# Kernel tuning notes

Hardware: AMD Instinct MI355X
Metric: run time of the kernel (lower is better)

The kernel has to match this reference:

```python
import jax, jax.numpy as jnp
import numpy as np

NF, NLOC, NNEI = 4, 2048, 64
EMBED, PAIR_DIM, H = 128, 64, 8
HD = EMBED // H
EPS = 1e-5

def _ln(x, g, b):
    m = x.mean(-1, keepdims=True)
    v = ((x - m) ** 2).mean(-1, keepdims=True)
    return (x - m) * jax.lax.rsqrt(v + EPS) * g + b

def setup_inputs() -> dict:
    key = jax.random.key(0)
    ks = jax.random.split(key, 12)
    inp = {
        "query": jax.random.normal(ks[0], (NF, NLOC, EMBED), jnp.float32),
        "pair": jax.random.normal(ks[1], (NF, NLOC, NNEI, PAIR_DIM), jnp.float32),
        "nlist": jax.random.randint(ks[2], (NF, NLOC, NNEI), 0, NLOC, jnp.int64),
        "delta_pos": jax.random.normal(ks[3], (NF, NLOC, NNEI, 3), jnp.float32),
        "attn_mask": jnp.zeros((NF, H, NLOC, NNEI), jnp.float32),
        "ln_g": jnp.ones((EMBED,), jnp.float32),
        "ln_b": jnp.zeros((EMBED,), jnp.float32),
        "pn_g": jnp.ones((PAIR_DIM,), jnp.float32),
        "pn_b": jnp.zeros((PAIR_DIM,), jnp.float32),
        "Wq": jax.random.normal(ks[4], (EMBED, EMBED), jnp.float32) * (EMBED ** -0.5),
        "Wk": jax.random.normal(ks[5], (EMBED, EMBED), jnp.float32) * (EMBED ** -0.5),
        "Wv": jax.random.normal(ks[6], (EMBED, EMBED), jnp.float32) * (EMBED ** -0.5),
        "Wbias": jax.random.normal(ks[7], (H, PAIR_DIM), jnp.float32) * (PAIR_DIM ** -0.5),
        "bbias": jnp.zeros((H,), jnp.float32),
        "Wforce": jax.random.normal(ks[8], (1, EMBED), jnp.float32) * (EMBED ** -0.5),
    }
    return inp

def reference(query, pair, nlist, delta_pos, attn_mask,
              ln_g, ln_b, pn_g, pn_b, Wq, Wk, Wv, Wbias, bbias, Wforce):
    nf, nloc, _ = query.shape
    nnei = nlist.shape[-1]
    qn = _ln(query, ln_g, ln_b)            # [f,l,e]
    pn = _ln(pair, pn_g, pn_b)             # [f,l,n,p]
    scaling = HD ** -0.5
    q = (qn @ Wq.T).reshape(nf, nloc, H, HD) * scaling       # [f,l,h,d]
    k = qn @ Wk.T                                            # [f,l,e]
    v = qn @ Wv.T
    idx = nlist.reshape(nf, -1)[..., None]                   # [f,l*n,1]
    kg = jnp.take_along_axis(k, idx, axis=1).reshape(nf, nloc, nnei, H, HD)
    vg = jnp.take_along_axis(v, idx, axis=1).reshape(nf, nloc, nnei, H, HD)
    attn = jnp.einsum('flhd,flnhd->fhln', q, kg)             # [f,h,l,n]
    bias = jnp.einsum('flnp,hp->fhln', pn, Wbias) + bbias[None, :, None, None]
    probs = jax.nn.softmax(attn + attn_mask + bias, axis=-1)  # dropout off (eval)
    # rotate by delta_pos and contract with v over neighbors
    x = jnp.einsum('fhln,flnc,flnhd->flchd', probs, delta_pos, vg)
    x = x.reshape(nf, nloc, 3, EMBED)
    force = (x @ Wforce.T).squeeze(-1)                       # [f,l,3]
    return force
```

## Files before the change

### kernel.cpp

```cpp
#include <hip/hip_runtime.h>

#define NFR   4
#define NLOCC 2048
#define NNEIN 64
#define EMB   128
#define PDIM  64
#define NH    8
#define LNEPS 1e-5f
#define NROW  (NFR*NLOCC)

#define WS_Q   0
#define WS_K   (NROW*EMB)
#define WS_FV  (2*NROW*EMB)
#define WS_WVF (2*NROW*EMB + NROW*NH)
#define WS_G   (WS_WVF + NH*EMB)
#define WS_SG  (WS_G + NH*PDIM)

__device__ __forceinline__ void fma4(float4& acc, const float4 a, const float4 b) {
    acc.x = fmaf(a.x, b.x, acc.x);
    acc.y = fmaf(a.y, b.y, acc.y);
    acc.z = fmaf(a.z, b.z, acc.z);
    acc.w = fmaf(a.w, b.w, acc.w);
}
__device__ __forceinline__ void fma4s(float4& acc, const float s, const float4 b) {
    acc.x = fmaf(s, b.x, acc.x);
    acc.y = fmaf(s, b.y, acc.y);
    acc.z = fmaf(s, b.z, acc.z);
    acc.w = fmaf(s, b.w, acc.w);
}
__device__ __forceinline__ float hsum4(const float4 a) {
    return (a.x + a.y) + (a.z + a.w);
}
__device__ __forceinline__ float dot4(const float4 a, const float4 b) {
    return fmaf(a.x, b.x, fmaf(a.y, b.y, fmaf(a.z, b.z, a.w * b.w)));
}
__device__ __forceinline__ float4 scale4(const float4 a, const float s) {
    return make_float4(a.x*s, a.y*s, a.z*s, a.w*s);
}

__global__ __launch_bounds__(256) void precompute_kernel(
    const float* __restrict__ pn_g, const float* __restrict__ pn_b,
    const float* __restrict__ Wbias, const float* __restrict__ bbias,
    const float* __restrict__ Wv, const float* __restrict__ Wforce,
    float* __restrict__ ws)
{
    const int t = threadIdx.x;
    {
        const int h  = t >> 5;
        const int e0 = (t & 31) * 4;
        float4 acc = make_float4(0.f, 0.f, 0.f, 0.f);
        #pragma unroll
        for (int d = 0; d < 16; ++d) {
            const float wf = Wforce[h*16 + d];
            const float4 wv = *(const float4*)(Wv + (size_t)(h*16 + d)*EMB + e0);
            fma4s(acc, wf, wv);
        }
        *(float4*)(ws + WS_WVF + (size_t)h*EMB + e0) = acc;
    }
    for (int idx = t; idx < NH*PDIM; idx += 256) {
        const int h = idx >> 6, p = idx & 63;
        ws[WS_G + idx] = pn_g[p] * Wbias[h*PDIM + p];
    }
    if (t < NH) {
        float sg = 0.f, c = 0.f;
        #pragma unroll 8
        for (int p = 0; p < PDIM; ++p) {
            const float wb = Wbias[t*PDIM + p];
            sg = fmaf(pn_g[p], wb, sg);
            c  = fmaf(pn_b[p], wb, c);
        }
        ws[WS_SG + t]      = sg;
        ws[WS_SG + NH + t] = c + bbias[t];
    }
}

__global__ __launch_bounds__(256, 2) void qkfv_kernel(
    const float* __restrict__ query,
    const float* __restrict__ ln_g, const float* __restrict__ ln_b,
    const float* __restrict__ Wq, const float* __restrict__ Wk,
    float* __restrict__ ws)
{
    __shared__ float gb_s[2][EMB];
    __shared__ float qn_s[16*132];
    __shared__ float wt_s[2][16*132];
    const int t = threadIdx.x;
    const int rowbase = blockIdx.x * 16;

    if (t < 64) {
        const float* src = (t < 32) ? ln_g : ln_b;
        ((float4*)gb_s[t >> 5])[t & 31] = ((const float4*)src)[t & 31];
    }

    const int r   = t >> 4;
    const int seg = t & 15;
    float4 x0 = ((const float4*)query)[(size_t)(rowbase + r)*32 + seg*2 + 0];
    float4 x1 = ((const float4*)query)[(size_t)(rowbase + r)*32 + seg*2 + 1];
    float s  = (x0.x + x0.y) + (x0.z + x0.w) + (x1.x + x1.y) + (x1.z + x1.w);
    float ss = x0.x*x0.x + x0.y*x0.y + x0.z*x0.z + x0.w*x0.w
             + x1.x*x1.x + x1.y*x1.y + x1.z*x1.z + x1.w*x1.w;
    #pragma unroll
    for (int m = 1; m < 16; m <<= 1) {
        s  += __shfl_xor(s,  m, 64);
        ss += __shfl_xor(ss, m, 64);
    }
    const float mean = s * (1.0f / 128.0f);
    const float var  = ss * (1.0f / 128.0f) - mean * mean;
    const float rstd = rsqrtf(var + LNEPS);
    __syncthreads();

    {
        const int c0 = seg * 8;
        float4 o0, o1;
        o0.x = (x0.x - mean)*rstd*gb_s[0][c0+0] + gb_s[1][c0+0];
        o0.y = (x0.y - mean)*rstd*gb_s[0][c0+1] + gb_s[1][c0+1];
        o0.z = (x0.z - mean)*rstd*gb_s[0][c0+2] + gb_s[1][c0+2];
        o0.w = (x0.w - mean)*rstd*gb_s[0][c0+3] + gb_s[1][c0+3];
        o1.x = (x1.x - mean)*rstd*gb_s[0][c0+4] + gb_s[1][c0+4];
        o1.y = (x1.y - mean)*rstd*gb_s[0][c0+5] + gb_s[1][c0+5];
        o1.z = (x1.z - mean)*rstd*gb_s[0][c0+6] + gb_s[1][c0+6];
        o1.w = (x1.w - mean)*rstd*gb_s[0][c0+7] + gb_s[1][c0+7];
        ((float4*)qn_s)[r*33 + seg*2 + 0] = o0;
        ((float4*)qn_s)[r*33 + seg*2 + 1] = o1;
    }
    __syncthreads();

    const int rp = t >> 5;
    const int r0 = rp * 2;
    const int cq = t & 31;
    const int sc0 = t >> 2;
    const int si0 = t & 3;
    const float4* qn4 = (const float4*)qn_s;

    for (int w = 0; w < 2; ++w) {
        const float4* W4 = (const float4*)((w == 0) ? Wq : Wk);
        float4 acc0 = make_float4(0.f,0.f,0.f,0.f);
        float4 acc1 = make_float4(0.f,0.f,0.f,0.f);
        {
            float4 g0 = W4[(size_t)sc0*32 + si0];
            float4 g1 = W4[(size_t)(sc0+64)*32 + si0];
            float* wt = wt_s[0];
            wt[(si0*4+0)*132 + sc0] = g0.x; wt[(si0*4+1)*132 + sc0] = g0.y;
            wt[(si0*4+2)*132 + sc0] = g0.z; wt[(si0*4+3)*132 + sc0] = g0.w;
            wt[(si0*4+0)*132 + sc0+64] = g1.x; wt[(si0*4+1)*132 + sc0+64] = g1.y;
            wt[(si0*4+2)*132 + sc0+64] = g1.z; wt[(si0*4+3)*132 + sc0+64] = g1.w;
        }
        __syncthreads();
        #pragma unroll
        for (int tau = 0; tau < 8; ++tau) {
            const int buf = tau & 1;
            float4 ng0, ng1;
            if (tau < 7) {
                ng0 = W4[(size_t)sc0*32 + (tau+1)*4 + si0];
                ng1 = W4[(size_t)(sc0+64)*32 + (tau+1)*4 + si0];
            }
            const float4* wt4 = (const float4*)wt_s[buf];
            #pragma unroll
            for (int e4 = 0; e4 < 4; ++e4) {
                float4 a0 = qn4[r0*33 + tau*4 + e4];
                float4 a1 = qn4[(r0+1)*33 + tau*4 + e4];
                const float* a0p = (const float*)&a0;
                const float* a1p = (const float*)&a1;
                #pragma unroll
                for (int ee = 0; ee < 4; ++ee) {
                    const float4 wv = wt4[(e4*4+ee)*33 + cq];
                    fma4s(acc0, a0p[ee], wv);
                    fma4s(acc1, a1p[ee], wv);
                }
            }
            if (tau < 7) {
                float* wt = wt_s[buf ^ 1];
                wt[(si0*4+0)*132 + sc0] = ng0.x; wt[(si0*4+1)*132 + sc0] = ng0.y;
                wt[(si0*4+2)*132 + sc0] = ng0.z; wt[(si0*4+3)*132 + sc0] = ng0.w;
                wt[(si0*4+0)*132 + sc0+64] = ng1.x; wt[(si0*4+1)*132 + sc0+64] = ng1.y;
                wt[(si0*4+2)*132 + sc0+64] = ng1.z; wt[(si0*4+3)*132 + sc0+64] = ng1.w;
            }
            __syncthreads();
        }
        const float sc = (w == 0) ? 0.25f : 1.0f;
        float4* dst = (float4*)(ws + (w == 0 ? WS_Q : WS_K));
        dst[(size_t)(rowbase + r0)*32 + cq]     = scale4(acc0, sc);
        dst[(size_t)(rowbase + r0 + 1)*32 + cq] = scale4(acc1, sc);
    }

    if (t < 128) {
        const int rr = t >> 3, h = t & 7;
        const float4* wvf4 = (const float4*)(ws + WS_WVF + (size_t)h*EMB);
        float4 acc = make_float4(0.f,0.f,0.f,0.f);
        #pragma unroll
        for (int ch = 0; ch < 32; ++ch)
            fma4(acc, qn4[rr*33 + ch], wvf4[ch]);
        ws[WS_FV + (size_t)(rowbase + rr)*NH + h] = hsum4(acc);
    }
}

__global__ __launch_bounds__(256, 4) void attn_force_kernel(
    const float* __restrict__ pair, const int* __restrict__ nlist,
    const float* __restrict__ delta_pos, const float* __restrict__ attn_mask,
    const float* __restrict__ ws, float* __restrict__ out)
{
    __shared__ float  logit_s[NNEIN*9];
    __shared__ float4 G_s4[128];
    __shared__ float  fpart[4][3];

    const int t    = threadIdx.x;
    const int bid  = blockIdx.x;
    const int fr   = bid >> 11;
    const int l    = bid & 2047;
    const int w    = t >> 6;
    const int lane = t & 63;
    const int half = lane >> 5;
    const int c    = lane & 31;
    const int n    = (w << 4) | (lane >> 2);
    const int sub  = lane & 3;
    const int h0   = sub * 2, h1 = h0 + 1;
    const int i32  = lane & 31;
    const int hh   = (w << 1) | half;

    const float4* prow = (const float4*)(pair + ((size_t)bid*NNEIN + n)*PDIM);
    float4 pr0 = prow[sub*4+0];
    float4 pr1 = prow[sub*4+1];
    float4 pr2 = prow[sub*4+2];
    float4 pr3 = prow[sub*4+3];

    const int jv = nlist[(size_t)bid*NNEIN + lane];
    const float4 q4c = ((const float4*)(ws + WS_Q))[(size_t)bid*32 + c];

    const float mask0 = attn_mask[((size_t)(fr*NH + h0)*NLOCC + l)*NNEIN + n];
    const float mask1 = attn_mask[((size_t)(fr*NH + h1)*NLOCC + l)*NNEIN + n];
    const float sg0 = ws[WS_SG + h0],      sg1 = ws[WS_SG + h1];
    const float cc0 = ws[WS_SG + NH + h0], cc1 = ws[WS_SG + NH + h1];

    const float* dpA = delta_pos + ((size_t)bid*NNEIN + i32)*3;
    const float* dpB = delta_pos + ((size_t)bid*NNEIN + i32 + 32)*3;
    const float dpax = dpA[0], dpay = dpA[1], dpaz = dpA[2];
    const float dpbx = dpB[0], dpby = dpB[1], dpbz = dpB[2];

    if (t < 128) G_s4[t] = ((const float4*)(ws + WS_G))[t];

    const int jA = __shfl(jv, i32, 64);
    const int jB = __shfl(jv, i32 + 32, 64);
    const float fvA = ws[WS_FV + ((size_t)(fr << 11) + jA)*NH + hh];
    const float fvB = ws[WS_FV + ((size_t)(fr << 11) + jB)*NH + hh];

    {
        const float4* k4 = (const float4*)(ws + WS_K) + (size_t)(fr << 11)*32;
        int jr[8];
        #pragma unroll
        for (int i = 0; i < 8; ++i)
            jr[i] = __shfl(jv, (w << 4) | (i << 1) | half, 64);
        float4 kkA[4], kkB[4];
        #pragma unroll
        for (int i = 0; i < 4; ++i) kkA[i] = k4[(size_t)jr[i]*32 + c];
        #pragma unroll
        for (int i = 0; i < 4; ++i) kkB[i] = k4[(size_t)jr[4+i]*32 + c];
        float p[8];
        #pragma unroll
        for (int i = 0; i < 4; ++i) p[i]     = dot4(kkA[i], q4c);
        #pragma unroll
        for (int i = 0; i < 4; ++i) p[4 + i] = dot4(kkB[i], q4c);
        #pragma unroll
        for (int i = 0; i < 8; ++i) {
            float pp = p[i];
            pp += __shfl_xor(pp, 1, 64);
            pp += __shfl_xor(pp, 2, 64);
            if ((c & 3) == 0)
                logit_s[((w << 4) | (i << 1) | half)*9 + (c >> 2)] = pp;
        }
    }
    __syncthreads();

    {
        float s  = hsum4(pr0) + hsum4(pr1) + hsum4(pr2) + hsum4(pr3);
        float ss = dot4(pr0, pr0) + dot4(pr1, pr1) + dot4(pr2, pr2) + dot4(pr3, pr3);
        s  += __shfl_xor(s, 1, 64);  s  += __shfl_xor(s, 2, 64);
        ss += __shfl_xor(ss, 1, 64); ss += __shfl_xor(ss, 2, 64);
        const float mean = s * (1.0f / 64.0f);
        const float var  = ss * (1.0f / 64.0f) - mean * mean;
        const float rstd = rsqrtf(var + LNEPS);

        float d[NH];
        #pragma unroll
        for (int h = 0; h < NH; ++h) d[h] = 0.f;
        const float4 prq[4] = {pr0, pr1, pr2, pr3};
        #pragma unroll
        for (int q = 0; q < 4; ++q) {
            #pragma unroll
            for (int h = 0; h < NH; ++h)
                d[h] += dot4(prq[q], G_s4[h*16 + sub*4 + q]);
        }
        #pragma unroll
        for (int h = 0; h < NH; ++h) {
            d[h] += __shfl_xor(d[h], 1, 64);
            d[h] += __shfl_xor(d[h], 2, 64);
        }
        const float b0 = rstd*(d[h0] - mean*sg0) + cc0 + mask0;
        const float b1 = rstd*(d[h1] - mean*sg1) + cc1 + mask1;
        logit_s[n*9 + h0] += b0;
        logit_s[n*9 + h1] += b1;
    }
    __syncthreads();

    {
        float a = logit_s[i32*9 + hh], b = logit_s[(i32 + 32)*9 + hh];
        float m = fmaxf(a, b);
        #pragma unroll
        for (int mm = 16; mm >= 1; mm >>= 1) m = fmaxf(m, __shfl_xor(m, mm, 64));
        float ea = __expf(a - m), eb = __expf(b - m);
        float sum = ea + eb;
        #pragma unroll
        for (int mm = 16; mm >= 1; mm >>= 1) sum += __shfl_xor(sum, mm, 64);
        const float inv = 1.0f / sum;
        float ca = ea * inv * fvA;
        float cb = eb * inv * fvB;
        ca += __shfl_xor(ca, 32, 64);
        cb += __shfl_xor(cb, 32, 64);
        float f0 = ca*dpax + cb*dpbx;
        float f1 = ca*dpay + cb*dpby;
        float f2 = ca*dpaz + cb*dpbz;
        #pragma unroll
        for (int mm = 1; mm <= 16; mm <<= 1) {
            f0 += __shfl_xor(f0, mm, 64);
            f1 += __shfl_xor(f1, mm, 64);
            f2 += __shfl_xor(f2, mm, 64);
        }
        if (lane == 0) {
            fpart[w][0] = f0; fpart[w][1] = f1; fpart[w][2] = f2;
        }
    }
    __syncthreads();

    if (t < 3)
        out[(size_t)bid*3 + t] = fpart[0][t] + fpart[1][t] + fpart[2][t] + fpart[3][t];
}

extern "C" void kernel_launch(void* const* d_in, const int* in_sizes, int n_in,
                              void* d_out, int out_size, void* d_ws, size_t ws_size,
                              hipStream_t stream) {
    const float* query     = (const float*)d_in[0];
    const float* pair      = (const float*)d_in[1];
    const int*   nlist     = (const int*)d_in[2];
    const float* delta_pos = (const float*)d_in[3];
    const float* attn_mask = (const float*)d_in[4];
    const float* ln_g      = (const float*)d_in[5];
    const float* ln_b      = (const float*)d_in[6];
    const float* pn_g      = (const float*)d_in[7];
    const float* pn_b      = (const float*)d_in[8];
    const float* Wq        = (const float*)d_in[9];
    const float* Wk        = (const float*)d_in[10];
    const float* Wv        = (const float*)d_in[11];
    const float* Wbias     = (const float*)d_in[12];
    const float* bbias     = (const float*)d_in[13];
    const float* Wforce    = (const float*)d_in[14];
    float* out = (float*)d_out;
    float* ws  = (float*)d_ws;

    precompute_kernel<<<1, 256, 0, stream>>>(pn_g, pn_b, Wbias, bbias, Wv, Wforce, ws);
    qkfv_kernel<<<512, 256, 0, stream>>>(query, ln_g, ln_b, Wq, Wk, ws);
    attn_force_kernel<<<NROW, 256, 0, stream>>>(pair, nlist, delta_pos, attn_mask, ws, out);
}
```

Baseline: 265.2 us.

## Stage pair rows and delta_pos through LDS with coalesced loads, restructure force reduction

Pair rows are now loaded with fully coalesced float4 reads across the whole block into a padded shared-memory tile, instead of strided per-thread row loads. delta_pos is staged in shared memory, and the value gather is done as one float2 per thread. Softmax probabilities are written back to LDS and the force reduction is remapped per neighbour, which costs an extra barrier. Shared-memory use grows by about 17 KB per block, which may reduce occupancy under launch_bounds(256,4).

```diff
diff --git a/kernel.cpp b/kernel.cpp
--- a/kernel.cpp
+++ b/kernel.cpp
@@ -198,8 +198,10 @@
     const float* __restrict__ delta_pos, const float* __restrict__ attn_mask,
     const float* __restrict__ ws, float* __restrict__ out)
 {
+    __shared__ float4 pair_s4[64*17];
     __shared__ float  logit_s[NNEIN*9];
     __shared__ float4 G_s4[128];
+    __shared__ float  dp_s[192];
     __shared__ float  fpart[4][3];
 
     const int t    = threadIdx.x;
@@ -210,18 +212,21 @@
     const int lane = t & 63;
     const int half = lane >> 5;
     const int c    = lane & 31;
-    const int n    = (w << 4) | (lane >> 2);
-    const int sub  = lane & 3;
+    const int n    = t >> 2;
+    const int sub  = t & 3;
     const int h0   = sub * 2, h1 = h0 + 1;
     const int i32  = lane & 31;
-    const int hh   = (w << 1) | half;
-
-    const float4* prow = (const float4*)(pair + ((size_t)bid*NNEIN + n)*PDIM);
-    float4 pr0 = prow[sub*4+0];
-    float4 pr1 = prow[sub*4+1];
-    float4 pr2 = prow[sub*4+2];
-    float4 pr3 = prow[sub*4+3];
-
+    const int hh   = t >> 5;
+
+    {
+        const float4* p4 = (const float4*)pair + (size_t)bid*1024;
+        #pragma unroll
+        for (int i = 0; i < 4; ++i) {
+            const int ci   = i*256 + t;
+            const float4 v = p4[ci];
+            pair_s4[(ci >> 4)*17 + (ci & 15)] = v;
+        }
+    }
     const int jv = nlist[(size_t)bid*NNEIN + lane];
     const float4 q4c = ((const float4*)(ws + WS_Q))[(size_t)bid*32 + c];
 
@@ -230,17 +235,11 @@
     const float sg0 = ws[WS_SG + h0],      sg1 = ws[WS_SG + h1];
     const float cc0 = ws[WS_SG + NH + h0], cc1 = ws[WS_SG + NH + h1];
 
-    const float* dpA = delta_pos + ((size_t)bid*NNEIN + i32)*3;
-    const float* dpB = delta_pos + ((size_t)bid*NNEIN + i32 + 32)*3;
-    const float dpax = dpA[0], dpay = dpA[1], dpaz = dpA[2];
-    const float dpbx = dpB[0], dpby = dpB[1], dpbz = dpB[2];
-
     if (t < 128) G_s4[t] = ((const float4*)(ws + WS_G))[t];
-
-    const int jA = __shfl(jv, i32, 64);
-    const int jB = __shfl(jv, i32 + 32, 64);
-    const float fvA = ws[WS_FV + ((size_t)(fr << 11) + jA)*NH + hh];
-    const float fvB = ws[WS_FV + ((size_t)(fr << 11) + jB)*NH + hh];
+    if (t < 48)  ((float4*)dp_s)[t] = ((const float4*)(delta_pos + (size_t)bid*192))[t];
+
+    const int    jn  = __shfl(jv, n & 63, 64);
+    const float2 fv2 = ((const float2*)(ws + WS_FV + ((size_t)(fr << 11) + jn)*NH))[sub];
 
     {
         const float4* k4 = (const float4*)(ws + WS_K) + (size_t)(fr << 11)*32;
@@ -270,6 +269,10 @@
     __syncthreads();
 
     {
+        const float4 pr0 = pair_s4[n*17 + sub*4 + 0];
+        const float4 pr1 = pair_s4[n*17 + sub*4 + 1];
+        const float4 pr2 = pair_s4[n*17 + sub*4 + 2];
+        const float4 pr3 = pair_s4[n*17 + sub*4 + 3];
         float s  = hsum4(pr0) + hsum4(pr1) + hsum4(pr2) + hsum4(pr3);
         float ss = dot4(pr0, pr0) + dot4(pr1, pr1) + dot4(pr2, pr2) + dot4(pr3, pr3);
         s  += __shfl_xor(s, 1, 64);  s  += __shfl_xor(s, 2, 64);
@@ -310,22 +313,22 @@
         #pragma unroll
         for (int mm = 16; mm >= 1; mm >>= 1) sum += __shfl_xor(sum, mm, 64);
         const float inv = 1.0f / sum;
-        float ca = ea * inv * fvA;
-        float cb = eb * inv * fvB;
-        ca += __shfl_xor(ca, 32, 64);
-        cb += __shfl_xor(cb, 32, 64);
-        float f0 = ca*dpax + cb*dpbx;
-        float f1 = ca*dpay + cb*dpby;
-        float f2 = ca*dpaz + cb*dpbz;
-        #pragma unroll
-        for (int mm = 1; mm <= 16; mm <<= 1) {
-            f0 += __shfl_xor(f0, mm, 64);
-            f1 += __shfl_xor(f1, mm, 64);
-            f2 += __shfl_xor(f2, mm, 64);
-        }
-        if (lane == 0) {
-            fpart[w][0] = f0; fpart[w][1] = f1; fpart[w][2] = f2;
-        }
+        logit_s[i32*9 + hh]        = ea * inv;
+        logit_s[(i32 + 32)*9 + hh] = eb * inv;
+    }
+    __syncthreads();
+
+    {
+        const float p0 = logit_s[n*9 + h0];
+        const float p1 = logit_s[n*9 + h1];
+        float sn = p0*fv2.x + p1*fv2.y;
+        sn += __shfl_xor(sn, 1, 64);
+        sn += __shfl_xor(sn, 2, 64);
+        float fc = (sub < 3) ? sn * dp_s[n*3 + sub] : 0.f;
+        #pragma unroll
+        for (int mm = 4; mm <= 32; mm <<= 1)
+            fc += __shfl_xor(fc, mm, 64);
+        if (lane < 3) fpart[w][lane] = fc;
     }
     __syncthreads();
 
```

Result: no change. 260.0 us (-1.9%).
